# Kernel optimization log

Measured on AMD Instinct MI355X. Metric: run time of the kernel, lower is better.

Reference implementation:

```python
import jax, jax.numpy as jnp
import numpy as np

NUM_HEADS = 16
HIDDEN = 1024
HEADSIZE = HIDDEN // NUM_HEADS


def setup_inputs() -> dict:
    key = jax.random.key(0)
    ks = jax.random.split(key, 9)
    B, S, H = 4, 2048, HIDDEN
    s = 1.0 / np.sqrt(H)
    return {
        "x": jax.random.normal(ks[0], (B, S, H), dtype=jnp.float32),
        "Wq": jax.random.normal(ks[1], (H, H), dtype=jnp.float32) * s,
        "bq": jax.random.normal(ks[2], (H,), dtype=jnp.float32) * s,
        "Wk": jax.random.normal(ks[3], (H, H), dtype=jnp.float32) * s,
        "bk": jax.random.normal(ks[4], (H,), dtype=jnp.float32) * s,
        "Wv": jax.random.normal(ks[5], (H, H), dtype=jnp.float32) * s,
        "bv": jax.random.normal(ks[6], (H,), dtype=jnp.float32) * s,
        "Wo": jax.random.normal(ks[7], (H, H), dtype=jnp.float32) * s,
        "bo": jax.random.normal(ks[8], (H,), dtype=jnp.float32) * s,
    }


def reference(x, Wq, bq, Wk, bk, Wv, bv, Wo, bo):
    B, S, H = x.shape
    nh, hs = NUM_HEADS, HEADSIZE

    def split_heads(y):  # (B,S,H) -> (B,nh,S,hs)
        return y.reshape(B, S, nh, hs).transpose(0, 2, 1, 3)

    q = split_heads(x @ Wq.T + bq)
    k = split_heads(x @ Wk.T + bk)
    v = split_heads(x @ Wv.T + bv)

    scores = jnp.einsum("bhqd,bhkd->bhqk", q, k) / jnp.sqrt(jnp.float32(hs))
    # causal mask: q_ind < k_ind gets -1e9 (matches torch.where(mask, -1e9, scores))
    q_ind = jnp.arange(S)[:, None]
    k_ind = jnp.arange(S)[None, :]
    scores = jnp.where(q_ind < k_ind, jnp.float32(-1e9), scores)
    attn = jax.nn.softmax(scores, axis=-1)
    out = jnp.einsum("bhqk,bhkd->bhqd", attn, v)  # (B,nh,S,hs)
    out = out.transpose(0, 2, 1, 3).reshape(B, S, H)
    return out @ Wo.T + bo
```

## Files before the change

kernel.cpp:

```cpp
#include <hip/hip_runtime.h>

#define NH 16
#define HS 64
#define HID 1024
#define SEQ 2048
#define BB 4
#define MR (BB*SEQ)
#define KD 1024
#define NT 32
#define QSCALE 0.18033688f

typedef __bf16 bf16;
typedef __attribute__((ext_vector_type(8))) __bf16 bf16x8;
typedef __attribute__((ext_vector_type(4))) __bf16 bf16x4;
typedef __attribute__((ext_vector_type(4))) float f32x4;
typedef __attribute__((ext_vector_type(16))) float f32x16;
typedef __attribute__((ext_vector_type(4))) float f4;
typedef __attribute__((ext_vector_type(2))) unsigned uintx2;

typedef __attribute__((address_space(3))) unsigned int as3u;
typedef __attribute__((address_space(1))) unsigned int as1u;

__device__ __forceinline__ void gl_lds16(const void* g, void* l) {
  __builtin_amdgcn_global_load_lds((const as1u*)g, (as3u*)l, 16, 0, 0);
}

__device__ __forceinline__ f32x4 mfma16(bf16x8 a, bf16x8 b, f32x4 c) {
  return __builtin_amdgcn_mfma_f32_16x16x32_bf16(a, b, c, 0, 0, 0);
}

__device__ __forceinline__ f32x16 mfma32(bf16x8 a, bf16x8 b, f32x16 c) {
  return __builtin_amdgcn_mfma_f32_32x32x16_bf16(a, b, c, 0, 0, 0);
}

__device__ __forceinline__ uintx2 plswap(unsigned a, unsigned b) {
#if __has_builtin(__builtin_amdgcn_permlane32_swap)
  return __builtin_amdgcn_permlane32_swap(a, b, false, false);
#else
  asm volatile("v_permlane32_swap_b32 %0, %1" : "+&v"(a), "+v"(b));
  uintx2 r; r[0] = a; r[1] = b; return r;
#endif
}

__device__ __forceinline__ float xmax32(float x) {
  uintx2 r = plswap(__float_as_uint(x), __float_as_uint(x));
  return fmaxf(__uint_as_float(r[0]), __uint_as_float(r[1]));
}
__device__ __forceinline__ float xadd32(float x) {
  uintx2 r = plswap(__float_as_uint(x), __float_as_uint(x));
  return __uint_as_float(r[0]) + __uint_as_float(r[1]);
}

__device__ __forceinline__ unsigned cvtpk(float lo, float hi) {
  unsigned r;
  asm("v_cvt_pk_bf16_f32 %0, %1, %2" : "=v"(r) : "v"(lo), "v"(hi));
  return r;
}

#define XN4   (MR*HID/4)
#define WN4   (HID*KD/4)
__global__ __launch_bounds__(256) void k_cvt_all(const float* __restrict__ x,
                                                 const float* __restrict__ w0, const float* __restrict__ w1,
                                                 const float* __restrict__ w2, const float* __restrict__ w3,
                                                 bf16* __restrict__ xb,
                                                 bf16* __restrict__ o0, bf16* __restrict__ o1,
                                                 bf16* __restrict__ o2, bf16* __restrict__ o3) {
  int i = blockIdx.x * 256 + threadIdx.x;
  const float* in; bf16* out; int j;
  if (i < XN4)            { in = x;  out = xb; j = i; }
  else if (i < XN4+WN4)   { in = w0; out = o0; j = i - XN4; }
  else if (i < XN4+2*WN4) { in = w1; out = o1; j = i - XN4 - WN4; }
  else if (i < XN4+3*WN4) { in = w2; out = o2; j = i - XN4 - 2*WN4; }
  else                    { in = w3; out = o3; j = i - XN4 - 3*WN4; }
  f4 v = reinterpret_cast<const f4*>(in)[j];
  bf16x4 h;
  h[0] = (bf16)v[0]; h[1] = (bf16)v[1]; h[2] = (bf16)v[2]; h[3] = (bf16)v[3];
  reinterpret_cast<bf16x4*>(out)[j] = h;
}

template<int MODE>
__global__ __launch_bounds__(512, 4) void k_gemm_p(const bf16* __restrict__ A,
                                                   const bf16* __restrict__ w0, const bf16* __restrict__ w1,
                                                   const bf16* __restrict__ w2,
                                                   const float* __restrict__ b0, const float* __restrict__ b1,
                                                   const float* __restrict__ b2p,
                                                   void* __restrict__ o0, void* __restrict__ o1,
                                                   void* __restrict__ o2) {
  __shared__ __align__(16) bf16 As[3][128*32];
  __shared__ __align__(16) bf16 Bs[3][256*32];
  const int tid = threadIdx.x, l = tid & 63, w = tid >> 6;
  const int wr = w >> 2, wc = w & 3;
  const int m0 = blockIdx.x * 128;
  const int ny = blockIdx.y;
  const int which = (MODE == 0) ? (ny >> 2) : 0;
  const int n0 = (MODE == 0) ? (ny & 3) * 256 : ny * 256;
  const bf16* Bw = (MODE == 1) ? w0 : (which == 0 ? w0 : which == 1 ? w1 : w2);
  const float* bias = (MODE == 1) ? b0 : (which == 0 ? b0 : which == 1 ? b1 : b2p);

  const int sra = tid >> 2;
  const int sca = (tid & 3) ^ ((sra >> 1) & 3);
  const bf16* Ag = A  + (size_t)(m0 + sra) * KD + sca * 8;
  const bf16* Bg = Bw + (size_t)(n0 + sra) * KD + sca * 8;

  gl_lds16(Ag,                        (char*)As[0] + w * 1024);
  gl_lds16(Bg,                        (char*)Bs[0] + w * 1024);
  gl_lds16(Bg + (size_t)128 * KD,     (char*)Bs[0] + 8192 + w * 1024);
  gl_lds16(Ag + 32,                   (char*)As[1] + w * 1024);
  gl_lds16(Bg + 32,                   (char*)Bs[1] + w * 1024);
  gl_lds16(Bg + (size_t)128 * KD + 32, (char*)Bs[1] + 8192 + w * 1024);

  f32x4 acc[4][4] = {};
  const int la = l & 15, lg = l >> 4;

  for (int t = 0; t < NT; ++t) {
    const int bq = t % 3;
    if (t < NT - 1) { asm volatile("s_waitcnt vmcnt(3)" ::: "memory"); }
    else            { asm volatile("s_waitcnt vmcnt(0)" ::: "memory"); }
    __builtin_amdgcn_sched_barrier(0);
    __builtin_amdgcn_s_barrier();
    __builtin_amdgcn_sched_barrier(0);

    bf16x8 af[4], bf_[2];
    #pragma unroll
    for (int mf = 0; mf < 4; mf++) {
      const int ra = wr * 64 + mf * 16 + la;
      const int ca = lg ^ ((ra >> 1) & 3);
      af[mf] = *(const bf16x8*)((const char*)As[bq] + ra * 64 + ca * 16);
    }
    #pragma unroll
    for (int nf = 0; nf < 2; nf++) {
      const int rb = wc * 64 + nf * 16 + la;
      const int cb = lg ^ ((rb >> 1) & 3);
      bf_[nf] = *(const bf16x8*)((const char*)Bs[bq] + rb * 64 + cb * 16);
    }
    const int t2 = t + 2;
    if (t2 < NT) {
      const int b2 = t2 % 3;
      gl_lds16(Ag + t2 * 32, (char*)As[b2] + w * 1024);
      gl_lds16(Bg + t2 * 32, (char*)Bs[b2] + w * 1024);
    }
    asm volatile("s_waitcnt lgkmcnt(0)" ::: "memory");
    __builtin_amdgcn_sched_barrier(0);
    __builtin_amdgcn_s_setprio(1);
    #pragma unroll
    for (int mf = 0; mf < 4; mf++) {
      acc[mf][0] = mfma16(af[mf], bf_[0], acc[mf][0]);
      acc[mf][1] = mfma16(af[mf], bf_[1], acc[mf][1]);
    }
    __builtin_amdgcn_s_setprio(0);

    #pragma unroll
    for (int nf = 0; nf < 2; nf++) {
      const int rb = wc * 64 + (nf + 2) * 16 + la;
      const int cb = lg ^ ((rb >> 1) & 3);
      bf_[nf] = *(const bf16x8*)((const char*)Bs[bq] + rb * 64 + cb * 16);
    }
    if (t2 < NT) {
      const int b2 = t2 % 3;
      gl_lds16(Bg + (size_t)128 * KD + t2 * 32, (char*)Bs[b2] + 8192 + w * 1024);
    }
    asm volatile("s_waitcnt lgkmcnt(0)" ::: "memory");
    __builtin_amdgcn_sched_barrier(0);
    __builtin_amdgcn_s_setprio(1);
    #pragma unroll
    for (int mf = 0; mf < 4; mf++) {
      acc[mf][2] = mfma16(af[mf], bf_[0], acc[mf][2]);
      acc[mf][3] = mfma16(af[mf], bf_[1], acc[mf][3]);
    }
    __builtin_amdgcn_s_setprio(0);
  }

  const float scale = (MODE == 0 && which == 0) ? QSCALE : 1.0f;
  #pragma unroll
  for (int mf = 0; mf < 4; mf++) {
    #pragma unroll
    for (int nf = 0; nf < 4; nf++) {
      const int n = n0 + wc * 64 + nf * 16 + la;
      const float bn = bias[n];
      #pragma unroll
      for (int j = 0; j < 4; j++) {
        const int m = m0 + wr * 64 + mf * 16 + lg * 4 + j;
        const float v = (acc[mf][nf][j] + bn) * scale;
        if (MODE == 0) {
          if (which == 2) {
            ((bf16*)o2)[(((size_t)(m >> 11) * NH + (n >> 6)) * HS + (n & 63)) * SEQ + (m & (SEQ - 1))] = (bf16)v;
          } else {
            bf16* dst = (which == 0) ? (bf16*)o0 : (bf16*)o1;
            dst[(((size_t)(m >> 11) * NH + (n >> 6)) * SEQ + (m & (SEQ - 1))) * HS + (n & 63)] = (bf16)v;
          }
        } else {
          ((float*)o0)[(size_t)m * HID + n] = v;
        }
      }
    }
  }
}

__global__ __launch_bounds__(256, 3) void k_gemm_o(const bf16* __restrict__ A,
                                                   const bf16* __restrict__ Bw,
                                                   const float* __restrict__ bias,
                                                   float* __restrict__ outp) {
  __shared__ __align__(16) bf16 As[3][128*32];
  __shared__ __align__(16) bf16 Bs[3][128*32];
  const int tid = threadIdx.x, l = tid & 63, w = tid >> 6;
  const int wr = w >> 1, wc = w & 1;
  const int m0 = blockIdx.x * 128;
  const int n0 = blockIdx.y * 128;

  const int sra = tid >> 2;
  const int sca = (tid & 3) ^ ((sra >> 1) & 3);
  const bf16* Ag = A  + (size_t)(m0 + sra) * KD + sca * 8;
  const bf16* Bg = Bw + (size_t)(n0 + sra) * KD + sca * 8;

  gl_lds16(Ag,                        (char*)As[0] + w * 1024);
  gl_lds16(Ag + (size_t)64 * KD,      (char*)As[0] + 4096 + w * 1024);
  gl_lds16(Bg,                        (char*)Bs[0] + w * 1024);
  gl_lds16(Bg + (size_t)64 * KD,      (char*)Bs[0] + 4096 + w * 1024);
  gl_lds16(Ag + 32,                   (char*)As[1] + w * 1024);
  gl_lds16(Ag + (size_t)64 * KD + 32, (char*)As[1] + 4096 + w * 1024);
  gl_lds16(Bg + 32,                   (char*)Bs[1] + w * 1024);
  gl_lds16(Bg + (size_t)64 * KD + 32, (char*)Bs[1] + 4096 + w * 1024);

  f32x4 acc[4][4] = {};
  const int la = l & 15, lg = l >> 4;

  for (int t = 0; t < NT; ++t) {
    const int bq = t % 3;
    if (t < NT - 1) { asm volatile("s_waitcnt vmcnt(4)" ::: "memory"); }
    else            { asm volatile("s_waitcnt vmcnt(0)" ::: "memory"); }
    __builtin_amdgcn_sched_barrier(0);
    __builtin_amdgcn_s_barrier();
    __builtin_amdgcn_sched_barrier(0);

    bf16x8 af[4], bf_[2];
    #pragma unroll
    for (int mf = 0; mf < 4; mf++) {
      const int ra = wr * 64 + mf * 16 + la;
      const int ca = lg ^ ((ra >> 1) & 3);
      af[mf] = *(const bf16x8*)((const char*)As[bq] + ra * 64 + ca * 16);
    }
    #pragma unroll
    for (int nf = 0; nf < 2; nf++) {
      const int rb = wc * 64 + nf * 16 + la;
      const int cb = lg ^ ((rb >> 1) & 3);
      bf_[nf] = *(const bf16x8*)((const char*)Bs[bq] + rb * 64 + cb * 16);
    }
    const int t2 = t + 2;
    if (t2 < NT) {
      const int b2 = t2 % 3;
      gl_lds16(Ag + t2 * 32,                   (char*)As[b2] + w * 1024);
      gl_lds16(Ag + (size_t)64 * KD + t2 * 32, (char*)As[b2] + 4096 + w * 1024);
    }
    asm volatile("s_waitcnt lgkmcnt(0)" ::: "memory");
    __builtin_amdgcn_sched_barrier(0);
    __builtin_amdgcn_s_setprio(1);
    #pragma unroll
    for (int mf = 0; mf < 4; mf++) {
      acc[mf][0] = mfma16(af[mf], bf_[0], acc[mf][0]);
      acc[mf][1] = mfma16(af[mf], bf_[1], acc[mf][1]);
    }
    __builtin_amdgcn_s_setprio(0);

    #pragma unroll
    for (int nf = 0; nf < 2; nf++) {
      const int rb = wc * 64 + (nf + 2) * 16 + la;
      const int cb = lg ^ ((rb >> 1) & 3);
      bf_[nf] = *(const bf16x8*)((const char*)Bs[bq] + rb * 64 + cb * 16);
    }
    if (t2 < NT) {
      const int b2 = t2 % 3;
      gl_lds16(Bg + t2 * 32,                   (char*)Bs[b2] + w * 1024);
      gl_lds16(Bg + (size_t)64 * KD + t2 * 32, (char*)Bs[b2] + 4096 + w * 1024);
    }
    asm volatile("s_waitcnt lgkmcnt(0)" ::: "memory");
    __builtin_amdgcn_sched_barrier(0);
    __builtin_amdgcn_s_setprio(1);
    #pragma unroll
    for (int mf = 0; mf < 4; mf++) {
      acc[mf][2] = mfma16(af[mf], bf_[0], acc[mf][2]);
      acc[mf][3] = mfma16(af[mf], bf_[1], acc[mf][3]);
    }
    __builtin_amdgcn_s_setprio(0);
  }

  #pragma unroll
  for (int mf = 0; mf < 4; mf++) {
    #pragma unroll
    for (int nf = 0; nf < 4; nf++) {
      const int n = n0 + wc * 64 + nf * 16 + la;
      const float bn = bias[n];
      #pragma unroll
      for (int j = 0; j < 4; j++) {
        const int m = m0 + wr * 64 + mf * 16 + lg * 4 + j;
        outp[(size_t)m * HID + n] = acc[mf][nf][j] + bn;
      }
    }
  }
}

__global__ __launch_bounds__(256, 3) void k_attn(const bf16* __restrict__ Q,
                                                 const bf16* __restrict__ K,
                                                 const bf16* __restrict__ Vt,
                                                 bf16* __restrict__ Aout) {
  const int bh = blockIdx.x;
  const int bx = blockIdx.y;
  const int tid = threadIdx.x, l = tid & 63, w = tid >> 6;
  const int hi = l >> 5;

  __shared__ __align__(16) bf16 Ks[3][64*64];
  __shared__ __align__(16) bf16 Vs[3][64*64];

  const bf16* Qg = Q  + (size_t)bh * SEQ * HS;
  const bf16* Kg = K  + (size_t)bh * SEQ * HS;
  const bf16* Vg = Vt + (size_t)bh * HS * SEQ;

  const int bb = bh >> 4, hh = bh & 15;
  const int sr  = tid >> 3;
  const int swz = ((tid & 7) ^ (sr & 7)) * 8;

  for (int pass = 0; pass < 2; ++pass) {
    const int p_ = pass ? (15 - bx) : bx;
    const int q0 = p_ * 128;
    const int nt = 2 * p_ + 2;

    bf16x8 qf[4];
    {
      const bf16* qrow = Qg + (size_t)(q0 + w*32 + (l & 31)) * HS + hi * 8;
      #pragma unroll
      for (int m = 0; m < 4; m++)
        qf[m] = *(const bf16x8*)(qrow + m * 16);
    }
    __builtin_amdgcn_sched_barrier(0);

    #pragma unroll
    for (int i = 0; i < 2; i++) {
      gl_lds16(Kg + (size_t)(32*i + sr) * HS + swz,  (char*)Ks[0] + i*4096 + w*1024);
      gl_lds16(Vg + (size_t)(32*i + sr) * SEQ + swz, (char*)Vs[0] + i*4096 + w*1024);
    }
    #pragma unroll
    for (int i = 0; i < 2; i++) {
      gl_lds16(Kg + (size_t)(64 + 32*i + sr) * HS + swz,  (char*)Ks[1] + i*4096 + w*1024);
      gl_lds16(Vg + (size_t)(32*i + sr) * SEQ + 64 + swz, (char*)Vs[1] + i*4096 + w*1024);
    }
    asm volatile("s_waitcnt vmcnt(4)" ::: "memory");
    __builtin_amdgcn_sched_barrier(0);
    __builtin_amdgcn_s_barrier();
    __builtin_amdgcn_sched_barrier(0);

    float m_r = -1e30f, l_r = 0.f;
    f32x16 o[2] = {};
    const int qmax = q0 + w*32 + 31;
    const int qg   = q0 + w*32 + (l & 31);

    int cur = 0;
    for (int kt = 0; kt < nt; ++kt) {
      const int k0 = kt * 64;

      if (kt + 2 < nt) {
        const int k2 = k0 + 128;
        const int b2 = (cur == 0) ? 2 : cur - 1;
        #pragma unroll
        for (int i = 0; i < 2; i++) {
          gl_lds16(Kg + (size_t)(k2 + 32*i + sr) * HS + swz,  (char*)Ks[b2] + i*4096 + w*1024);
          gl_lds16(Vg + (size_t)(32*i + sr) * SEQ + k2 + swz, (char*)Vs[b2] + i*4096 + w*1024);
        }
      }

      if (k0 <= qmax) {
        f32x16 p[2] = {};
        #pragma unroll
        for (int b = 0; b < 2; b++) {
          #pragma unroll
          for (int m = 0; m < 4; m++) {
            const int row = 32*b + (l & 31);
            const int cc = 2*m + hi;
            bf16x8 kf = *(const bf16x8*)((const char*)Ks[cur] + row*128 + ((cc ^ (row & 7))*16));
            p[b] = mfma32(kf, qf[m], p[b]);
          }
        }

        if (k0 + 63 > q0 + w*32) {
          #pragma unroll
          for (int b = 0; b < 2; b++)
            #pragma unroll
            for (int r = 0; r < 16; r++) {
              const int kg = k0 + 32*b + (r & 3) + 8*(r >> 2) + 4*hi;
              if (kg > qg) p[b][r] = -1e30f;
            }
        }

        float rloc = -1e30f;
        #pragma unroll
        for (int b = 0; b < 2; b++)
          #pragma unroll
          for (int r = 0; r < 16; r++) rloc = fmaxf(rloc, p[b][r]);
        const float rmax = xmax32(rloc);

        if (__any(rmax > m_r + 8.0f)) {
          const float mn = fmaxf(m_r, rmax);
          const float alpha = __builtin_amdgcn_exp2f(m_r - mn);
          m_r = mn;
          l_r *= alpha;
          #pragma unroll
          for (int r = 0; r < 16; r++) {
            const float ar = __shfl(alpha, (r & 3) + 8*(r >> 2) + 4*hi);
            o[0][r] *= ar; o[1][r] *= ar;
          }
        }

        float sloc = 0.f;
        #pragma unroll
        for (int b = 0; b < 2; b++)
          #pragma unroll
          for (int r = 0; r < 16; r++) {
            const float e = __builtin_amdgcn_exp2f(p[b][r] - m_r);
            p[b][r] = e;
            sloc += e;
          }
        l_r += xadd32(sloc);

        bf16x8 pa[4];
        #pragma unroll
        for (int c = 0; c < 4; c++) {
          const int b = c >> 1, R = (c & 1) * 8;
          unsigned w01 = cvtpk(p[b][R+0], p[b][R+1]);
          unsigned w23 = cvtpk(p[b][R+2], p[b][R+3]);
          unsigned w89 = cvtpk(p[b][R+4], p[b][R+5]);
          unsigned wab = cvtpk(p[b][R+6], p[b][R+7]);
          uintx2 s1 = plswap(w01, w89);
          uintx2 s2 = plswap(w23, wab);
          union { unsigned u[4]; bf16x8 v; } uu;
          uu.u[0] = s1[0]; uu.u[1] = s2[0]; uu.u[2] = s1[1]; uu.u[3] = s2[1];
          pa[c] = uu.v;
        }

        #pragma unroll
        for (int d = 0; d < 2; d++) {
          #pragma unroll
          for (int c = 0; c < 4; c++) {
            const int row = 32*d + (l & 31);
            const int cc = 2*c + hi;
            bf16x8 vf = *(const bf16x8*)((const char*)Vs[cur] + row*128 + ((cc ^ (row & 7))*16));
            o[d] = mfma32(pa[c], vf, o[d]);
          }
        }
      }

      if (kt + 2 < nt) { asm volatile("s_waitcnt vmcnt(4)" ::: "memory"); }
      else             { asm volatile("s_waitcnt vmcnt(0)" ::: "memory"); }
      __builtin_amdgcn_sched_barrier(0);
      __builtin_amdgcn_s_barrier();
      __builtin_amdgcn_sched_barrier(0);
      cur = (cur == 2) ? 0 : cur + 1;
    }

    const float inv = 1.0f / l_r;
    #pragma unroll
    for (int r = 0; r < 16; r++) {
      const int qr = (r & 3) + 8*(r >> 2) + 4*hi;
      const float ir = __shfl(inv, qr);
      const int q = q0 + w*32 + qr;
      #pragma unroll
      for (int d = 0; d < 2; d++)
        Aout[(size_t)(bb*SEQ + q)*HID + hh*HS + d*32 + (l & 31)] = (bf16)(o[d][r] * ir);
    }
  }
}

extern "C" void kernel_launch(void* const* d_in, const int* in_sizes, int n_in,
                              void* d_out, int out_size, void* d_ws, size_t ws_size,
                              hipStream_t stream) {
  const float* x  = (const float*)d_in[0];
  const float* Wq = (const float*)d_in[1];
  const float* bq = (const float*)d_in[2];
  const float* Wk = (const float*)d_in[3];
  const float* bk = (const float*)d_in[4];
  const float* Wv = (const float*)d_in[5];
  const float* bv = (const float*)d_in[6];
  const float* Wo = (const float*)d_in[7];
  const float* bo = (const float*)d_in[8];

  char* ws = (char*)d_ws;
  const size_t MB = 1024 * 1024;
  bf16* xb  = (bf16*)(ws);
  bf16* wqb = (bf16*)(ws + 16*MB);
  bf16* wkb = (bf16*)(ws + 18*MB);
  bf16* wvb = (bf16*)(ws + 20*MB);
  bf16* wob = (bf16*)(ws + 22*MB);
  bf16* Qb  = (bf16*)(ws + 24*MB);
  bf16* Kb  = (bf16*)(ws + 40*MB);
  bf16* Vb  = (bf16*)(ws + 56*MB);
  bf16* Ab  = xb;

  k_cvt_all<<<(XN4 + 4*WN4 + 255)/256, 256, 0, stream>>>(x, Wq, Wk, Wv, Wo, xb, wqb, wkb, wvb, wob);

  k_gemm_p<0><<<dim3(MR/128, 12), 512, 0, stream>>>(xb, wqb, wkb, wvb, bq, bk, bv, Qb, Kb, Vb);

  k_attn<<<dim3(BB*NH, 8), 256, 0, stream>>>(Qb, Kb, Vb, Ab);

  k_gemm_o<<<dim3(MR/128, 8), 256, 0, stream>>>(Ab, wob, bo, (float*)d_out);
}
```

Measured before the change: 168.2 us.

## Rewrite QKV projection GEMM with BK=64 double-buffered quadrant-split pipeline

```diff
diff --git a/kernel.cpp b/kernel.cpp
--- a/kernel.cpp
+++ b/kernel.cpp
@@ -8,6 +8,7 @@
 #define MR (BB*SEQ)
 #define KD 1024
 #define NT 32
+#define NTG 16
 #define QSCALE 0.18033688f
 
 typedef __bf16 bf16;
@@ -78,118 +79,159 @@
   reinterpret_cast<bf16x4*>(out)[j] = h;
 }
 
-template<int MODE>
-__global__ __launch_bounds__(512, 4) void k_gemm_p(const bf16* __restrict__ A,
-                                                   const bf16* __restrict__ w0, const bf16* __restrict__ w1,
-                                                   const bf16* __restrict__ w2,
-                                                   const float* __restrict__ b0, const float* __restrict__ b1,
-                                                   const float* __restrict__ b2p,
-                                                   void* __restrict__ o0, void* __restrict__ o1,
-                                                   void* __restrict__ o2) {
-  __shared__ __align__(16) bf16 As[3][128*32];
-  __shared__ __align__(16) bf16 Bs[3][256*32];
+__global__ __launch_bounds__(512, 2) void k_gemm_q8(const bf16* __restrict__ A,
+                                                    const bf16* __restrict__ w0, const bf16* __restrict__ w1,
+                                                    const bf16* __restrict__ w2,
+                                                    const float* __restrict__ b0, const float* __restrict__ b1,
+                                                    const float* __restrict__ b2p,
+                                                    bf16* __restrict__ o0, bf16* __restrict__ o1,
+                                                    bf16* __restrict__ o2) {
+  __shared__ __align__(16) bf16 As[2][128*64];
+  __shared__ __align__(16) bf16 Bs[2][256*64];
   const int tid = threadIdx.x, l = tid & 63, w = tid >> 6;
-  const int wr = w >> 2, wc = w & 3;
+  const int wm = w >> 2, wn = w & 3;
   const int m0 = blockIdx.x * 128;
   const int ny = blockIdx.y;
-  const int which = (MODE == 0) ? (ny >> 2) : 0;
-  const int n0 = (MODE == 0) ? (ny & 3) * 256 : ny * 256;
-  const bf16* Bw = (MODE == 1) ? w0 : (which == 0 ? w0 : which == 1 ? w1 : w2);
-  const float* bias = (MODE == 1) ? b0 : (which == 0 ? b0 : which == 1 ? b1 : b2p);
-
-  const int sra = tid >> 2;
-  const int sca = (tid & 3) ^ ((sra >> 1) & 3);
-  const bf16* Ag = A  + (size_t)(m0 + sra) * KD + sca * 8;
-  const bf16* Bg = Bw + (size_t)(n0 + sra) * KD + sca * 8;
-
-  gl_lds16(Ag,                        (char*)As[0] + w * 1024);
-  gl_lds16(Bg,                        (char*)Bs[0] + w * 1024);
-  gl_lds16(Bg + (size_t)128 * KD,     (char*)Bs[0] + 8192 + w * 1024);
-  gl_lds16(Ag + 32,                   (char*)As[1] + w * 1024);
-  gl_lds16(Bg + 32,                   (char*)Bs[1] + w * 1024);
-  gl_lds16(Bg + (size_t)128 * KD + 32, (char*)Bs[1] + 8192 + w * 1024);
+  const int which = ny >> 2;
+  const int n0 = (ny & 3) * 256;
+  const bf16* Bw = (which == 0) ? w0 : (which == 1) ? w1 : w2;
+  const float* bias = (which == 0) ? b0 : (which == 1) ? b1 : b2p;
+
+  const int u = tid >> 3;
+  const int cg = (tid & 7) ^ (u & 7);
+  const bf16* Ags = A + (size_t)(m0 + (u >> 5) * 64 + (u & 31)) * KD + cg * 8;
+  const bf16* Bgs = Bw + (size_t)(n0 + (u >> 5) * 64 + (u & 31)) * KD + cg * 8;
+
+#define STAGE_A(buf, t, h) \
+  gl_lds16(Ags + (size_t)(h) * 32 * KD + (t) * 64, (char*)As[buf] + (h) * 8192 + tid * 16)
+#define STAGE_B(buf, t, hb) \
+  gl_lds16(Bgs + (size_t)(((hb) & 1) * 128 + ((hb) >> 1) * 32) * KD + (t) * 64, \
+           (char*)Bs[buf] + (hb) * 8192 + tid * 16)
+
+  STAGE_A(0, 0, 0); STAGE_B(0, 0, 0); STAGE_B(0, 0, 1);
+  STAGE_A(0, 0, 1); STAGE_B(0, 0, 2); STAGE_B(0, 0, 3);
+  asm volatile("s_waitcnt vmcnt(0)" ::: "memory");
+  __builtin_amdgcn_sched_barrier(0);
+  __builtin_amdgcn_s_barrier();
+  __builtin_amdgcn_sched_barrier(0);
 
   f32x4 acc[4][4] = {};
   const int la = l & 15, lg = l >> 4;
-
-  for (int t = 0; t < NT; ++t) {
-    const int bq = t % 3;
-    if (t < NT - 1) { asm volatile("s_waitcnt vmcnt(3)" ::: "memory"); }
-    else            { asm volatile("s_waitcnt vmcnt(0)" ::: "memory"); }
+  bf16x8 af0[2][2], af1[2][2], bf[2][2];
+
+#define RD_A(dst, mh, f, ks) { \
+    const int row = (mh) * 64 + wm * 32 + (f) * 16 + la; \
+    const int ch = ((ks) * 4 + lg) ^ (row & 7); \
+    dst = *(const bf16x8*)((const char*)As[cb] + row * 128 + ch * 16); }
+#define RD_B(dst, nh, nf_, ks) { \
+    const int row = (nh) * 128 + wn * 32 + (nf_) * 16 + la; \
+    const int ch = ((ks) * 4 + lg) ^ (row & 7); \
+    dst = *(const bf16x8*)((const char*)Bs[cb] + row * 128 + ch * 16); }
+
+  for (int t = 0; t < NTG; ++t) {
+    const int cb = t & 1, nb = cb ^ 1;
+    const bool st = (t + 1) < NTG;
+
+    if (t > 0) {
+      asm volatile("s_waitcnt vmcnt(3)" ::: "memory");
+      __builtin_amdgcn_sched_barrier(0);
+      __builtin_amdgcn_s_barrier();
+      __builtin_amdgcn_sched_barrier(0);
+    }
+    #pragma unroll
+    for (int f = 0; f < 2; f++)
+      #pragma unroll
+      for (int ks = 0; ks < 2; ks++) RD_A(af0[f][ks], 0, f, ks);
+    #pragma unroll
+    for (int nf_ = 0; nf_ < 2; nf_++)
+      #pragma unroll
+      for (int ks = 0; ks < 2; ks++) RD_B(bf[nf_][ks], 0, nf_, ks);
+    if (st) { STAGE_A(nb, t + 1, 0); STAGE_B(nb, t + 1, 0); }
+    asm volatile("s_waitcnt lgkmcnt(0)" ::: "memory");
+    __builtin_amdgcn_sched_barrier(0);
+    __builtin_amdgcn_s_setprio(1);
+    #pragma unroll
+    for (int f = 0; f < 2; f++)
+      #pragma unroll
+      for (int nf_ = 0; nf_ < 2; nf_++)
+        #pragma unroll
+        for (int ks = 0; ks < 2; ks++)
+          acc[f][nf_] = mfma16(af0[f][ks], bf[nf_][ks], acc[f][nf_]);
+    __builtin_amdgcn_s_setprio(0);
+
+    if (st) { asm volatile("s_waitcnt vmcnt(4)" ::: "memory"); }
+    else    { asm volatile("s_waitcnt vmcnt(2)" ::: "memory"); }
     __builtin_amdgcn_sched_barrier(0);
     __builtin_amdgcn_s_barrier();
     __builtin_amdgcn_sched_barrier(0);
-
-    bf16x8 af[4], bf_[2];
-    #pragma unroll
-    for (int mf = 0; mf < 4; mf++) {
-      const int ra = wr * 64 + mf * 16 + la;
-      const int ca = lg ^ ((ra >> 1) & 3);
-      af[mf] = *(const bf16x8*)((const char*)As[bq] + ra * 64 + ca * 16);
-    }
-    #pragma unroll
-    for (int nf = 0; nf < 2; nf++) {
-      const int rb = wc * 64 + nf * 16 + la;
-      const int cb = lg ^ ((rb >> 1) & 3);
-      bf_[nf] = *(const bf16x8*)((const char*)Bs[bq] + rb * 64 + cb * 16);
-    }
-    const int t2 = t + 2;
-    if (t2 < NT) {
-      const int b2 = t2 % 3;
-      gl_lds16(Ag + t2 * 32, (char*)As[b2] + w * 1024);
-      gl_lds16(Bg + t2 * 32, (char*)Bs[b2] + w * 1024);
-    }
+    #pragma unroll
+    for (int f = 0; f < 2; f++)
+      #pragma unroll
+      for (int ks = 0; ks < 2; ks++) RD_A(af1[f][ks], 1, f, ks);
+    if (st) { STAGE_B(nb, t + 1, 1); STAGE_A(nb, t + 1, 1); }
     asm volatile("s_waitcnt lgkmcnt(0)" ::: "memory");
     __builtin_amdgcn_sched_barrier(0);
     __builtin_amdgcn_s_setprio(1);
     #pragma unroll
-    for (int mf = 0; mf < 4; mf++) {
-      acc[mf][0] = mfma16(af[mf], bf_[0], acc[mf][0]);
-      acc[mf][1] = mfma16(af[mf], bf_[1], acc[mf][1]);
-    }
+    for (int f = 0; f < 2; f++)
+      #pragma unroll
+      for (int nf_ = 0; nf_ < 2; nf_++)
+        #pragma unroll
+        for (int ks = 0; ks < 2; ks++)
+          acc[2 + f][nf_] = mfma16(af1[f][ks], bf[nf_][ks], acc[2 + f][nf_]);
     __builtin_amdgcn_s_setprio(0);
 
-    #pragma unroll
-    for (int nf = 0; nf < 2; nf++) {
-      const int rb = wc * 64 + (nf + 2) * 16 + la;
-      const int cb = lg ^ ((rb >> 1) & 3);
-      bf_[nf] = *(const bf16x8*)((const char*)Bs[bq] + rb * 64 + cb * 16);
-    }
-    if (t2 < NT) {
-      const int b2 = t2 % 3;
-      gl_lds16(Bg + (size_t)128 * KD + t2 * 32, (char*)Bs[b2] + 8192 + w * 1024);
-    }
+    if (st) { asm volatile("s_waitcnt vmcnt(4)" ::: "memory"); }
+    else    { asm volatile("s_waitcnt vmcnt(0)" ::: "memory"); }
+    __builtin_amdgcn_sched_barrier(0);
+    __builtin_amdgcn_s_barrier();
+    __builtin_amdgcn_sched_barrier(0);
+    #pragma unroll
+    for (int nf_ = 0; nf_ < 2; nf_++)
+      #pragma unroll
+      for (int ks = 0; ks < 2; ks++) RD_B(bf[nf_][ks], 1, nf_, ks);
+    if (st) { STAGE_B(nb, t + 1, 2); STAGE_B(nb, t + 1, 3); }
     asm volatile("s_waitcnt lgkmcnt(0)" ::: "memory");
     __builtin_amdgcn_sched_barrier(0);
     __builtin_amdgcn_s_setprio(1);
     #pragma unroll
-    for (int mf = 0; mf < 4; mf++) {
-      acc[mf][2] = mfma16(af[mf], bf_[0], acc[mf][2]);
-      acc[mf][3] = mfma16(af[mf], bf_[1], acc[mf][3]);
-    }
+    for (int f = 0; f < 2; f++)
+      #pragma unroll
+      for (int nf_ = 0; nf_ < 2; nf_++)
+        #pragma unroll
+        for (int ks = 0; ks < 2; ks++)
+          acc[2 + f][2 + nf_] = mfma16(af1[f][ks], bf[nf_][ks], acc[2 + f][2 + nf_]);
+
+    #pragma unroll
+    for (int f = 0; f < 2; f++)
+      #pragma unroll
+      for (int nf_ = 0; nf_ < 2; nf_++)
+        #pragma unroll
+        for (int ks = 0; ks < 2; ks++)
+          acc[f][2 + nf_] = mfma16(af0[f][ks], bf[nf_][ks], acc[f][2 + nf_]);
     __builtin_amdgcn_s_setprio(0);
   }
-
-  const float scale = (MODE == 0 && which == 0) ? QSCALE : 1.0f;
+#undef RD_A
+#undef RD_B
+#undef STAGE_A
+#undef STAGE_B
+
+  const float scale = (which == 0) ? QSCALE : 1.0f;
   #pragma unroll
   for (int mf = 0; mf < 4; mf++) {
     #pragma unroll
     for (int nf = 0; nf < 4; nf++) {
-      const int n = n0 + wc * 64 + nf * 16 + la;
+      const int n = n0 + wn * 64 + nf * 16 + la;
       const float bn = bias[n];
       #pragma unroll
       for (int j = 0; j < 4; j++) {
-        const int m = m0 + wr * 64 + mf * 16 + lg * 4 + j;
+        const int m = m0 + wm * 64 + mf * 16 + lg * 4 + j;
         const float v = (acc[mf][nf][j] + bn) * scale;
-        if (MODE == 0) {
-          if (which == 2) {
-            ((bf16*)o2)[(((size_t)(m >> 11) * NH + (n >> 6)) * HS + (n & 63)) * SEQ + (m & (SEQ - 1))] = (bf16)v;
-          } else {
-            bf16* dst = (which == 0) ? (bf16*)o0 : (bf16*)o1;
-            dst[(((size_t)(m >> 11) * NH + (n >> 6)) * SEQ + (m & (SEQ - 1))) * HS + (n & 63)] = (bf16)v;
-          }
+        if (which == 2) {
+          o2[(((size_t)(m >> 11) * NH + (n >> 6)) * HS + (n & 63)) * SEQ + (m & (SEQ - 1))] = (bf16)v;
         } else {
-          ((float*)o0)[(size_t)m * HID + n] = v;
+          bf16* dst = (which == 0) ? o0 : o1;
+          dst[(((size_t)(m >> 11) * NH + (n >> 6)) * SEQ + (m & (SEQ - 1))) * HS + (n & 63)] = (bf16)v;
         }
       }
     }
@@ -340,7 +382,7 @@
     #pragma unroll
     for (int i = 0; i < 2; i++) {
       gl_lds16(Kg + (size_t)(64 + 32*i + sr) * HS + swz,  (char*)Ks[1] + i*4096 + w*1024);
-      gl_lds16(Vg + (size_t)(32*i + sr) * SEQ + 64 + swz, (char*)Vs[1] + i*4096 + w*1024);
+      gl_lds16(Vg + (size_t)sr * SEQ + 64 + 32*i*SEQ + swz, (char*)Vs[1] + i*4096 + w*1024);
     }
     asm volatile("s_waitcnt vmcnt(4)" ::: "memory");
     __builtin_amdgcn_sched_barrier(0);
@@ -494,7 +536,7 @@
 
   k_cvt_all<<<(XN4 + 4*WN4 + 255)/256, 256, 0, stream>>>(x, Wq, Wk, Wv, Wo, xb, wqb, wkb, wvb, wob);
 
-  k_gemm_p<0><<<dim3(MR/128, 12), 512, 0, stream>>>(xb, wqb, wkb, wvb, bq, bk, bv, Qb, Kb, Vb);
+  k_gemm_q8<<<dim3(MR/128, 12), 512, 0, stream>>>(xb, wqb, wkb, wvb, bq, bk, bv, Qb, Kb, Vb);
 
   k_attn<<<dim3(BB*NH, 8), 256, 0, stream>>>(Qb, Kb, Vb, Ab);
 
```

Measured after the change: 176.0 us. 1.05x slower.
